# Performance work log

Hardware: AMD Instinct MI355X
Metric: run time of the kernel (lower is better)

Reference implementation:

```python
import jax, jax.numpy as jnp
import numpy as np

TEMPERATURE = 0.5  # init temperature; attn_drop=0.0 so dropout is identity


def setup_inputs() -> dict:
    key = jax.random.key(0)
    k1, k2, k3 = jax.random.split(key, 3)
    B, H, N, D = 4, 8, 2048, 64
    q = jax.random.normal(k1, (B, H, N, D), dtype=jnp.float32)
    k = jax.random.normal(k2, (B, H, N, D), dtype=jnp.float32)
    v = jax.random.normal(k3, (B, H, N, D), dtype=jnp.float32)
    scale = jnp.asarray(D ** -0.5, dtype=jnp.float32)
    return {"q": q, "k": k, "v": v, "scale": scale}


def reference(q, k, v, scale):
    # logits: [B,H,N,N]
    logits = jnp.einsum("bhqd,bhkd->bhqk", q, k) * scale
    # first softmax acts as a soft mask over keys
    soft_mask = jax.nn.softmax(logits / TEMPERATURE, axis=-1)
    # second softmax over masked logits (elementwise product, NOT matmul)
    attn = jax.nn.softmax(logits * soft_mask, axis=-1)
    # dropout with p=0.0 is identity
    out = jnp.einsum("bhqk,bhkd->bhqd", attn, v)
    return out
```

## Files before the change

kernel.cpp:

```cpp
#include <hip/hip_runtime.h>


typedef _Float16 f16;
typedef f16 f16x8 __attribute__((ext_vector_type(8)));
typedef float f32x4 __attribute__((ext_vector_type(4)));

#define MFMA(a, b, c) __builtin_amdgcn_mfma_f32_16x16x32_f16((a), (b), (c), 0, 0, 0)
#define EXP2(x) __builtin_amdgcn_exp2f(x)

#define N_CTX 2048
#define DH 64
#define KT 64
#define NKT (N_CTX / KT)
#define ROWS 128
#define QS 72
#define HEAD_ELEMS (N_CTX * DH)

#define C2 2.885390081777927f

__device__ inline unsigned pk(float a, float b) {
    typedef __fp16 fp16x2_t __attribute__((ext_vector_type(2)));
    union { fp16x2_t v; unsigned u; } x;
    x.v = __builtin_amdgcn_cvt_pkrtz(a, b);
    return x.u;
}

__device__ inline void load16_lds(const f16* g, f16* l) {
    __builtin_amdgcn_global_load_lds(
        (const __attribute__((address_space(1))) void*)g,
        (__attribute__((address_space(3))) void*)l, 16, 0, 0);
}

__global__ __launch_bounds__(256)
void cvt_k(const float* __restrict__ k, f16* __restrict__ out) {
    int i = (blockIdx.x * 256 + threadIdx.x) * 8;
    float4 a = *(const float4*)&k[i];
    float4 b = *(const float4*)&k[i + 4];
    uint4 r = make_uint4(pk(a.x, a.y), pk(a.z, a.w), pk(b.x, b.y), pk(b.z, b.w));
    *(uint4*)&out[i] = r;
}

__global__ __launch_bounds__(256)
void cvt_vt(const float* __restrict__ v, f16* __restrict__ out) {
    __shared__ float Vs[64][65];
    const int bh = blockIdx.x >> 5;
    const int kt = blockIdx.x & 31;
    const int t  = threadIdx.x;
    const float* vb = v + (size_t)bh * HEAD_ELEMS + (size_t)kt * KT * DH;
    #pragma unroll
    for (int it = 0; it < 4; ++it) {
        int idx = it * 256 + t;
        int row = idx >> 4, c4 = idx & 15;
        float4 x = *(const float4*)&vb[row * DH + c4 * 4];
        *(float4*)&Vs[row][c4 * 4] = x;
    }
    __syncthreads();
    int d = t >> 2, kq = t & 3;
    unsigned w[8];
    #pragma unroll
    for (int j = 0; j < 8; ++j)
        w[j] = pk(Vs[kq * 16 + 2 * j][d], Vs[kq * 16 + 2 * j + 1][d]);
    f16* ob = out + (size_t)bh * HEAD_ELEMS + (size_t)d * N_CTX + kt * KT + kq * 16;
    *(uint4*)(ob)     = make_uint4(w[0], w[1], w[2], w[3]);
    *(uint4*)(ob + 8) = make_uint4(w[4], w[5], w[6], w[7]);
}

__global__ __launch_bounds__(512, 4)
void stk_attn_mfma(const float* __restrict__ qg, const f16* __restrict__ kh,
                   const f16* __restrict__ vth, const float* __restrict__ sg,
                   float* __restrict__ og) {
    __shared__ f16 Qs[ROWS * QS];
    __shared__ f16 Ks[2][KT * DH];
    __shared__ f16 Vt[2][DH * KT];
    __shared__ f16 Ps[8][16 * QS];

    const int tid  = threadIdx.x;
    const int wv   = tid >> 6;
    const int lane = tid & 63;
    const int l15  = lane & 15;
    const int q4   = lane >> 4;
    const int bh   = blockIdx.x & 31;
    const int q0   = (blockIdx.x >> 5) * ROWS;
    const float scale2 = sg[0] * C2;

    const float* qb = qg + (size_t)bh * HEAD_ELEMS;
    const f16*   kb = kh + (size_t)bh * HEAD_ELEMS;
    const f16*   vtb = vth + (size_t)bh * HEAD_ELEMS;
    float*       ob = og + (size_t)bh * HEAD_ELEMS;

    #pragma unroll
    for (int it = 0; it < 4; ++it) {
        int idx = it * 512 + tid;
        int row = idx >> 4, c4 = idx & 15;
        float4 v = *(const float4*)&qb[((size_t)(q0 + row)) * DH + c4 * 4];
        *(uint2*)&Qs[row * QS + c4 * 4] =
            make_uint2(pk(v.x * scale2, v.y * scale2), pk(v.z * scale2, v.w * scale2));
    }
    __syncthreads();

    f16x8 aq[2];
    #pragma unroll
    for (int kc = 0; kc < 2; ++kc)
        aq[kc] = *(const f16x8*)&Qs[(wv * 16 + l15) * QS + kc * 32 + q4 * 8];

    const int kc_   = wv * 64 + lane;
    const int kkey  = kc_ >> 3;
    const int kdl   = (kc_ & 7) ^ (kkey & 7);
    const int ks_src = kkey * DH + kdl * 8;
    const long vt_src = (long)kkey * N_CTX + kdl * 8;
    f16* const ks_dst0 = &Ks[0][wv * 512];
    f16* const vt_dst0 = &Vt[0][wv * 512];
    const int ko0 = l15 * 64 + ((q4 ^ (l15 & 7)) * 8);
    const int ko1 = l15 * 64 + (((q4 + 4) ^ (l15 & 7)) * 8);
    const int vo0 = l15 * 64 + ((q4 ^ (l15 & 7)) * 8);
    const int vo1 = l15 * 64 + (((4 + q4) ^ (l15 & 7)) * 8);
    f16* const ps_w = &Ps[wv][(q4 * 4) * QS + l15];
    const f16* const ps_r = &Ps[wv][l15 * QS + q4 * 8];

    float s1[4] = {0, 0, 0, 0};
    load16_lds(kb + ks_src, ks_dst0);
    __syncthreads();
    for (int kt = 0; kt < NKT; ++kt) {
        const int cur = kt & 1;
        if (kt + 1 < NKT)
            load16_lds(kb + (kt + 1) * (KT * DH) + ks_src, ks_dst0 + (cur ^ 1) * (KT * DH));
        #pragma unroll
        for (int kgi = 0; kgi < 4; ++kgi) {
            f16x8 b0 = *(const f16x8*)&Ks[cur][kgi * 1024 + ko0];
            f16x8 b1 = *(const f16x8*)&Ks[cur][kgi * 1024 + ko1];
            f32x4 acc = {0.f, 0.f, 0.f, 0.f};
            acc = MFMA(aq[0], b0, acc);
            acc = MFMA(aq[1], b1, acc);
            #pragma unroll
            for (int r = 0; r < 4; ++r)
                s1[r] += EXP2(acc[r]);
        }
        __syncthreads();
    }
    float inv1[4];
    #pragma unroll
    for (int s = 0; s < 4; ++s) {
        float v = s1[s];
        v += __shfl_xor(v, 1, 64);
        v += __shfl_xor(v, 2, 64);
        v += __shfl_xor(v, 4, 64);
        v += __shfl_xor(v, 8, 64);
        inv1[s] = 0.5f / v;
    }

    float l2[4] = {0, 0, 0, 0};
    f32x4 O[4];
    #pragma unroll
    for (int dt = 0; dt < 4; ++dt) O[dt] = (f32x4){0.f, 0.f, 0.f, 0.f};

    load16_lds(kb + ks_src, ks_dst0);
    load16_lds(vtb + vt_src, vt_dst0);
    __syncthreads();
    for (int kt = 0; kt < NKT; ++kt) {
        const int cur = kt & 1;
        if (kt + 1 < NKT) {
            load16_lds(kb + (kt + 1) * (KT * DH) + ks_src, ks_dst0 + (cur ^ 1) * (KT * DH));
            load16_lds(vtb + vt_src + (kt + 1) * KT, vt_dst0 + (cur ^ 1) * (DH * KT));
        }
        #pragma unroll
        for (int kgi = 0; kgi < 4; ++kgi) {
            f16x8 b0 = *(const f16x8*)&Ks[cur][kgi * 1024 + ko0];
            f16x8 b1 = *(const f16x8*)&Ks[cur][kgi * 1024 + ko1];
            f32x4 acc = {0.f, 0.f, 0.f, 0.f};
            acc = MFMA(aq[0], b0, acc);
            acc = MFMA(aq[1], b1, acc);
            #pragma unroll
            for (int r = 0; r < 4; ++r) {
                float a  = acc[r];
                float e1 = EXP2(a);
                float e2 = EXP2((a * e1) * inv1[r]);
                l2[r] += e2;
                ps_w[r * QS + kgi * 16] = (f16)e2;
            }
        }
        #pragma unroll
        for (int kc = 0; kc < 2; ++kc) {
            f16x8 ap = *(const f16x8*)&ps_r[kc * 32];
            const int vo = (kc == 0) ? vo0 : vo1;
            #pragma unroll
            for (int dt = 0; dt < 4; ++dt) {
                f16x8 bv = *(const f16x8*)&Vt[cur][dt * 1024 + vo];
                O[dt] = MFMA(ap, bv, O[dt]);
            }
        }
        __syncthreads();
    }

    float invl2[4];
    #pragma unroll
    for (int s = 0; s < 4; ++s) {
        float v = l2[s];
        v += __shfl_xor(v, 1, 64);
        v += __shfl_xor(v, 2, 64);
        v += __shfl_xor(v, 4, 64);
        v += __shfl_xor(v, 8, 64);
        invl2[s] = 1.0f / v;
    }
    #pragma unroll
    for (int dt = 0; dt < 4; ++dt)
        #pragma unroll
        for (int r = 0; r < 4; ++r) {
            int row = q0 + wv * 16 + q4 * 4 + r;
            ob[(size_t)row * DH + dt * 16 + l15] = O[dt][r] * invl2[r];
        }
}

extern "C" void kernel_launch(void* const* d_in, const int* in_sizes, int n_in,
                              void* d_out, int out_size, void* d_ws, size_t ws_size,
                              hipStream_t stream) {
    const float* q = (const float*)d_in[0];
    const float* k = (const float*)d_in[1];
    const float* v = (const float*)d_in[2];
    const float* s = (const float*)d_in[3];
    float* out = (float*)d_out;
    f16* kf = (f16*)d_ws;
    f16* vtf = (f16*)((char*)d_ws + 8388608);
    cvt_k<<<2048, 256, 0, stream>>>(k, kf);
    cvt_vt<<<1024, 256, 0, stream>>>(v, vtf);
    dim3 grid(32 * 16);
    stk_attn_mfma<<<grid, 512, 0, stream>>>(q, kf, vtf, s, out);
}
```

Baseline: 175.9 us.

## Switch attention to 32x32x16 MFMA with 4 waves of 32 rows, fuse K/V conversion

Rewrites the main attention kernel to use 32x32x16 MFMA tiles, with each of 4 waves handling 32 query rows instead of 8 waves of 16 rows. This cuts B-operand LDS reads per FLOP and amortizes K/V tile loads over more rows per wave. It also merges the K conversion and V transpose kernels into one launch with a permuted V layout that matches the new P layout. Register pressure rises (16-wide accumulators and per-row statistics), which may reduce occupancy.

```diff
diff --git a/kernel.cpp b/kernel.cpp
--- a/kernel.cpp
+++ b/kernel.cpp
@@ -3,9 +3,9 @@
 
 typedef _Float16 f16;
 typedef f16 f16x8 __attribute__((ext_vector_type(8)));
-typedef float f32x4 __attribute__((ext_vector_type(4)));
-
-#define MFMA(a, b, c) __builtin_amdgcn_mfma_f32_16x16x32_f16((a), (b), (c), 0, 0, 0)
+typedef float f32x16 __attribute__((ext_vector_type(16)));
+
+#define MFMA32(a, b, c) __builtin_amdgcn_mfma_f32_32x32x16_f16((a), (b), (c), 0, 0, 0)
 #define EXP2(x) __builtin_amdgcn_exp2f(x)
 
 #define N_CTX 2048
@@ -15,7 +15,6 @@
 #define ROWS 128
 #define QS 72
 #define HEAD_ELEMS (N_CTX * DH)
-
 #define C2 2.885390081777927f
 
 __device__ inline unsigned pk(float a, float b) {
@@ -32,53 +31,55 @@
 }
 
 __global__ __launch_bounds__(256)
-void cvt_k(const float* __restrict__ k, f16* __restrict__ out) {
-    int i = (blockIdx.x * 256 + threadIdx.x) * 8;
-    float4 a = *(const float4*)&k[i];
-    float4 b = *(const float4*)&k[i + 4];
-    uint4 r = make_uint4(pk(a.x, a.y), pk(a.z, a.w), pk(b.x, b.y), pk(b.z, b.w));
-    *(uint4*)&out[i] = r;
-}
-
-__global__ __launch_bounds__(256)
-void cvt_vt(const float* __restrict__ v, f16* __restrict__ out) {
+void cvt_kv(const float* __restrict__ k, const float* __restrict__ v,
+            f16* __restrict__ ko, f16* __restrict__ vto) {
     __shared__ float Vs[64][65];
-    const int bh = blockIdx.x >> 5;
-    const int kt = blockIdx.x & 31;
+    const int bh = blockIdx.x & 31;
+    const int kt = blockIdx.x >> 5;
     const int t  = threadIdx.x;
+    const float* kb = k + (size_t)bh * HEAD_ELEMS + (size_t)kt * KT * DH;
+    f16* kob = ko + (size_t)bh * HEAD_ELEMS + (size_t)kt * KT * DH;
+    #pragma unroll
+    for (int it = 0; it < 2; ++it) {
+        int i = (it * 256 + t) * 8;
+        float4 a = *(const float4*)&kb[i];
+        float4 b = *(const float4*)&kb[i + 4];
+        *(uint4*)&kob[i] = make_uint4(pk(a.x, a.y), pk(a.z, a.w), pk(b.x, b.y), pk(b.z, b.w));
+    }
     const float* vb = v + (size_t)bh * HEAD_ELEMS + (size_t)kt * KT * DH;
     #pragma unroll
     for (int it = 0; it < 4; ++it) {
         int idx = it * 256 + t;
         int row = idx >> 4, c4 = idx & 15;
-        float4 x = *(const float4*)&vb[row * DH + c4 * 4];
-        *(float4*)&Vs[row][c4 * 4] = x;
-    }
-    __syncthreads();
-    int d = t >> 2, kq = t & 3;
+        *(float4*)&Vs[row][c4 * 4] = *(const float4*)&vb[row * DH + c4 * 4];
+    }
+    __syncthreads();
+    int d = t >> 2, sub = t & 3;
     unsigned w[8];
     #pragma unroll
-    for (int j = 0; j < 8; ++j)
-        w[j] = pk(Vs[kq * 16 + 2 * j][d], Vs[kq * 16 + 2 * j + 1][d]);
-    f16* ob = out + (size_t)bh * HEAD_ELEMS + (size_t)d * N_CTX + kt * KT + kq * 16;
+    for (int j = 0; j < 8; ++j) {
+        int c = sub * 8 + j;
+        w[j] = pk(Vs[c][d], Vs[c + 32][d]);
+    }
+    f16* ob = vto + (size_t)bh * HEAD_ELEMS + (size_t)d * N_CTX + kt * KT + sub * 16;
     *(uint4*)(ob)     = make_uint4(w[0], w[1], w[2], w[3]);
     *(uint4*)(ob + 8) = make_uint4(w[4], w[5], w[6], w[7]);
 }
 
-__global__ __launch_bounds__(512, 4)
+__global__ __launch_bounds__(256, 2)
 void stk_attn_mfma(const float* __restrict__ qg, const f16* __restrict__ kh,
                    const f16* __restrict__ vth, const float* __restrict__ sg,
                    float* __restrict__ og) {
     __shared__ f16 Qs[ROWS * QS];
     __shared__ f16 Ks[2][KT * DH];
     __shared__ f16 Vt[2][DH * KT];
-    __shared__ f16 Ps[8][16 * QS];
+    __shared__ f16 Ps[4][32 * QS];
 
     const int tid  = threadIdx.x;
     const int wv   = tid >> 6;
     const int lane = tid & 63;
-    const int l15  = lane & 15;
-    const int q4   = lane >> 4;
+    const int l31  = lane & 31;
+    const int lh   = lane >> 5;
     const int bh   = blockIdx.x & 31;
     const int q0   = (blockIdx.x >> 5) * ROWS;
     const float scale2 = sg[0] * C2;
@@ -89,8 +90,8 @@
     float*       ob = og + (size_t)bh * HEAD_ELEMS;
 
     #pragma unroll
-    for (int it = 0; it < 4; ++it) {
-        int idx = it * 512 + tid;
+    for (int it = 0; it < 8; ++it) {
+        int idx = it * 256 + tid;
         int row = idx >> 4, c4 = idx & 15;
         float4 v = *(const float4*)&qb[((size_t)(q0 + row)) * DH + c4 * 4];
         *(uint2*)&Qs[row * QS + c4 * 4] =
@@ -98,116 +99,133 @@
     }
     __syncthreads();
 
-    f16x8 aq[2];
-    #pragma unroll
-    for (int kc = 0; kc < 2; ++kc)
-        aq[kc] = *(const f16x8*)&Qs[(wv * 16 + l15) * QS + kc * 32 + q4 * 8];
-
-    const int kc_   = wv * 64 + lane;
-    const int kkey  = kc_ >> 3;
-    const int kdl   = (kc_ & 7) ^ (kkey & 7);
-    const int ks_src = kkey * DH + kdl * 8;
-    const long vt_src = (long)kkey * N_CTX + kdl * 8;
-    f16* const ks_dst0 = &Ks[0][wv * 512];
-    f16* const vt_dst0 = &Vt[0][wv * 512];
-    const int ko0 = l15 * 64 + ((q4 ^ (l15 & 7)) * 8);
-    const int ko1 = l15 * 64 + (((q4 + 4) ^ (l15 & 7)) * 8);
-    const int vo0 = l15 * 64 + ((q4 ^ (l15 & 7)) * 8);
-    const int vo1 = l15 * 64 + (((4 + q4) ^ (l15 & 7)) * 8);
-    f16* const ps_w = &Ps[wv][(q4 * 4) * QS + l15];
-    const f16* const ps_r = &Ps[wv][l15 * QS + q4 * 8];
-
-    float s1[4] = {0, 0, 0, 0};
-    load16_lds(kb + ks_src, ks_dst0);
+    f16x8 aq[4];
+    #pragma unroll
+    for (int km = 0; km < 4; ++km)
+        aq[km] = *(const f16x8*)&Qs[(wv * 32 + l31) * QS + km * 16 + lh * 8];
+
+    const int c0   = (wv * 2) * 64 + lane;
+    const int c1   = c0 + 64;
+    const int key0 = c0 >> 3, key1 = c1 >> 3;
+    const int ks_src0 = key0 * DH + (((c0 & 7) ^ (key0 & 7)) * 8);
+    const int ks_src1 = key1 * DH + (((c1 & 7) ^ (key1 & 7)) * 8);
+    const long vt_src0 = (long)key0 * N_CTX + (((c0 & 7) ^ (key0 & 7)) * 8);
+    const long vt_src1 = (long)key1 * N_CTX + (((c1 & 7) ^ (key1 & 7)) * 8);
+    const int dst0 = (wv * 2) * 512, dst1 = dst0 + 512;
+    const int x8 = l31 & 7;
+    int xo[4];
+    #pragma unroll
+    for (int km = 0; km < 4; ++km) xo[km] = ((2 * km + lh) ^ x8) * 8;
+    const int gb0 = l31 * 64, gb1 = (32 + l31) * 64;
+    f16* const ps_wv = &Ps[wv][0];
+
+    float s1[16] = {0};
+    load16_lds(kb + ks_src0, &Ks[0][dst0]);
+    load16_lds(kb + ks_src1, &Ks[0][dst1]);
     __syncthreads();
     for (int kt = 0; kt < NKT; ++kt) {
         const int cur = kt & 1;
-        if (kt + 1 < NKT)
-            load16_lds(kb + (kt + 1) * (KT * DH) + ks_src, ks_dst0 + (cur ^ 1) * (KT * DH));
-        #pragma unroll
-        for (int kgi = 0; kgi < 4; ++kgi) {
-            f16x8 b0 = *(const f16x8*)&Ks[cur][kgi * 1024 + ko0];
-            f16x8 b1 = *(const f16x8*)&Ks[cur][kgi * 1024 + ko1];
-            f32x4 acc = {0.f, 0.f, 0.f, 0.f};
-            acc = MFMA(aq[0], b0, acc);
-            acc = MFMA(aq[1], b1, acc);
+        if (kt + 1 < NKT) {
+            const f16* src = kb + (kt + 1) * (KT * DH);
+            load16_lds(src + ks_src0, &Ks[cur ^ 1][dst0]);
+            load16_lds(src + ks_src1, &Ks[cur ^ 1][dst1]);
+        }
+        #pragma unroll
+        for (int kg = 0; kg < 2; ++kg) {
+            const int gb = kg ? gb1 : gb0;
+            f32x16 acc;
             #pragma unroll
-            for (int r = 0; r < 4; ++r)
+            for (int i = 0; i < 16; ++i) acc[i] = 0.f;
+            #pragma unroll
+            for (int km = 0; km < 4; ++km) {
+                f16x8 b = *(const f16x8*)&Ks[cur][gb + xo[km]];
+                acc = MFMA32(aq[km], b, acc);
+            }
+            #pragma unroll
+            for (int r = 0; r < 16; ++r)
                 s1[r] += EXP2(acc[r]);
         }
         __syncthreads();
     }
-    float inv1[4];
-    #pragma unroll
-    for (int s = 0; s < 4; ++s) {
-        float v = s1[s];
+    float inv1[16];
+    #pragma unroll
+    for (int r = 0; r < 16; ++r) {
+        float v = s1[r];
         v += __shfl_xor(v, 1, 64);
         v += __shfl_xor(v, 2, 64);
         v += __shfl_xor(v, 4, 64);
         v += __shfl_xor(v, 8, 64);
-        inv1[s] = 0.5f / v;
-    }
-
-    float l2[4] = {0, 0, 0, 0};
-    f32x4 O[4];
-    #pragma unroll
-    for (int dt = 0; dt < 4; ++dt) O[dt] = (f32x4){0.f, 0.f, 0.f, 0.f};
-
-    load16_lds(kb + ks_src, ks_dst0);
-    load16_lds(vtb + vt_src, vt_dst0);
+        v += __shfl_xor(v, 16, 64);
+        inv1[r] = 0.5f / v;
+    }
+
+    float l2[16] = {0};
+    f32x16 O0, O1;
+    #pragma unroll
+    for (int i = 0; i < 16; ++i) { O0[i] = 0.f; O1[i] = 0.f; }
+
+    load16_lds(kb + ks_src0, &Ks[0][dst0]);
+    load16_lds(kb + ks_src1, &Ks[0][dst1]);
+    load16_lds(vtb + vt_src0, &Vt[0][dst0]);
+    load16_lds(vtb + vt_src1, &Vt[0][dst1]);
     __syncthreads();
     for (int kt = 0; kt < NKT; ++kt) {
         const int cur = kt & 1;
         if (kt + 1 < NKT) {
-            load16_lds(kb + (kt + 1) * (KT * DH) + ks_src, ks_dst0 + (cur ^ 1) * (KT * DH));
-            load16_lds(vtb + vt_src + (kt + 1) * KT, vt_dst0 + (cur ^ 1) * (DH * KT));
-        }
-        #pragma unroll
-        for (int kgi = 0; kgi < 4; ++kgi) {
-            f16x8 b0 = *(const f16x8*)&Ks[cur][kgi * 1024 + ko0];
-            f16x8 b1 = *(const f16x8*)&Ks[cur][kgi * 1024 + ko1];
-            f32x4 acc = {0.f, 0.f, 0.f, 0.f};
-            acc = MFMA(aq[0], b0, acc);
-            acc = MFMA(aq[1], b1, acc);
-            #pragma unroll
-            for (int r = 0; r < 4; ++r) {
-                float a  = acc[r];
-                float e1 = EXP2(a);
-                float e2 = EXP2((a * e1) * inv1[r]);
-                l2[r] += e2;
-                ps_w[r * QS + kgi * 16] = (f16)e2;
-            }
-        }
-        #pragma unroll
-        for (int kc = 0; kc < 2; ++kc) {
-            f16x8 ap = *(const f16x8*)&ps_r[kc * 32];
-            const int vo = (kc == 0) ? vo0 : vo1;
-            #pragma unroll
-            for (int dt = 0; dt < 4; ++dt) {
-                f16x8 bv = *(const f16x8*)&Vt[cur][dt * 1024 + vo];
-                O[dt] = MFMA(ap, bv, O[dt]);
-            }
+            const f16* src = kb + (kt + 1) * (KT * DH);
+            load16_lds(src + ks_src0, &Ks[cur ^ 1][dst0]);
+            load16_lds(src + ks_src1, &Ks[cur ^ 1][dst1]);
+            load16_lds(vtb + vt_src0 + (kt + 1) * KT, &Vt[cur ^ 1][dst0]);
+            load16_lds(vtb + vt_src1 + (kt + 1) * KT, &Vt[cur ^ 1][dst1]);
+        }
+        f32x16 a0, a1;
+        #pragma unroll
+        for (int i = 0; i < 16; ++i) { a0[i] = 0.f; a1[i] = 0.f; }
+        #pragma unroll
+        for (int km = 0; km < 4; ++km) {
+            f16x8 b0 = *(const f16x8*)&Ks[cur][gb0 + xo[km]];
+            f16x8 b1 = *(const f16x8*)&Ks[cur][gb1 + xo[km]];
+            a0 = MFMA32(aq[km], b0, a0);
+            a1 = MFMA32(aq[km], b1, a1);
+        }
+        #pragma unroll
+        for (int r = 0; r < 16; ++r) {
+            int row_r = (r & 3) + 8 * (r >> 2) + 4 * lh;
+            float e10 = EXP2(a0[r]);
+            float e20 = EXP2((a0[r] * e10) * inv1[r]);
+            float e11 = EXP2(a1[r]);
+            float e21 = EXP2((a1[r] * e11) * inv1[r]);
+            l2[r] += e20 + e21;
+            *(unsigned*)&ps_wv[row_r * QS + 2 * l31] = pk(e20, e21);
+        }
+        #pragma unroll
+        for (int km = 0; km < 4; ++km) {
+            f16x8 ap = *(const f16x8*)&ps_wv[l31 * QS + km * 16 + lh * 8];
+            f16x8 bv0 = *(const f16x8*)&Vt[cur][gb0 + xo[km]];
+            f16x8 bv1 = *(const f16x8*)&Vt[cur][gb1 + xo[km]];
+            O0 = MFMA32(ap, bv0, O0);
+            O1 = MFMA32(ap, bv1, O1);
         }
         __syncthreads();
     }
 
-    float invl2[4];
-    #pragma unroll
-    for (int s = 0; s < 4; ++s) {
-        float v = l2[s];
+    float invl2[16];
+    #pragma unroll
+    for (int r = 0; r < 16; ++r) {
+        float v = l2[r];
         v += __shfl_xor(v, 1, 64);
         v += __shfl_xor(v, 2, 64);
         v += __shfl_xor(v, 4, 64);
         v += __shfl_xor(v, 8, 64);
-        invl2[s] = 1.0f / v;
-    }
-    #pragma unroll
-    for (int dt = 0; dt < 4; ++dt)
-        #pragma unroll
-        for (int r = 0; r < 4; ++r) {
-            int row = q0 + wv * 16 + q4 * 4 + r;
-            ob[(size_t)row * DH + dt * 16 + l15] = O[dt][r] * invl2[r];
-        }
+        v += __shfl_xor(v, 16, 64);
+        invl2[r] = 1.0f / v;
+    }
+    #pragma unroll
+    for (int r = 0; r < 16; ++r) {
+        int row = q0 + wv * 32 + (r & 3) + 8 * (r >> 2) + 4 * lh;
+        ob[(size_t)row * DH + l31]      = O0[r] * invl2[r];
+        ob[(size_t)row * DH + 32 + l31] = O1[r] * invl2[r];
+    }
 }
 
 extern "C" void kernel_launch(void* const* d_in, const int* in_sizes, int n_in,
@@ -218,10 +236,9 @@
     const float* v = (const float*)d_in[2];
     const float* s = (const float*)d_in[3];
     float* out = (float*)d_out;
-    f16* kf = (f16*)d_ws;
+    f16* kf  = (f16*)d_ws;
     f16* vtf = (f16*)((char*)d_ws + 8388608);
-    cvt_k<<<2048, 256, 0, stream>>>(k, kf);
-    cvt_vt<<<1024, 256, 0, stream>>>(v, vtf);
+    cvt_kv<<<1024, 256, 0, stream>>>(k, v, kf, vtf);
     dim3 grid(32 * 16);
-    stk_attn_mfma<<<grid, 512, 0, stream>>>(q, kf, vtf, s, out);
-}
+    stk_attn_mfma<<<grid, 256, 0, stream>>>(q, kf, vtf, s, out);
+}
```

Result: no change. 177.5 us (+0.9%).

## Software-pipeline QK MFMAs one tile ahead and fuse K/V conversion kernels

Applied to the files above, without the earlier changes.

Both passes now compute the QK^T MFMA tile for the next key block before doing the exp/softmax work on the current one, so matrix-core work overlaps with the transcendental VALU work. K tiles are prefetched two ahead into the double buffer. The separate K-convert and V-transpose kernels are merged into one launch, removing one kernel launch. This costs extra accumulator registers (accN/accC), which may pressure occupancy under launch_bounds(512,4).

```diff
diff --git a/kernel.cpp b/kernel.cpp
--- a/kernel.cpp
+++ b/kernel.cpp
@@ -14,8 +14,8 @@
 #define NKT (N_CTX / KT)
 #define ROWS 128
 #define QS 72
+#define KTDH (KT * DH)
 #define HEAD_ELEMS (N_CTX * DH)
-
 #define C2 2.885390081777927f
 
 __device__ inline unsigned pk(float a, float b) {
@@ -32,35 +32,35 @@
 }
 
 __global__ __launch_bounds__(256)
-void cvt_k(const float* __restrict__ k, f16* __restrict__ out) {
-    int i = (blockIdx.x * 256 + threadIdx.x) * 8;
-    float4 a = *(const float4*)&k[i];
-    float4 b = *(const float4*)&k[i + 4];
-    uint4 r = make_uint4(pk(a.x, a.y), pk(a.z, a.w), pk(b.x, b.y), pk(b.z, b.w));
-    *(uint4*)&out[i] = r;
-}
-
-__global__ __launch_bounds__(256)
-void cvt_vt(const float* __restrict__ v, f16* __restrict__ out) {
+void cvt_kv(const float* __restrict__ k, const float* __restrict__ v,
+            f16* __restrict__ ko, f16* __restrict__ vto) {
     __shared__ float Vs[64][65];
-    const int bh = blockIdx.x >> 5;
-    const int kt = blockIdx.x & 31;
+    const int bh = blockIdx.x & 31;
+    const int kt = blockIdx.x >> 5;
     const int t  = threadIdx.x;
+    const float* kb = k + (size_t)bh * HEAD_ELEMS + (size_t)kt * KT * DH;
+    f16* kob = ko + (size_t)bh * HEAD_ELEMS + (size_t)kt * KT * DH;
+    #pragma unroll
+    for (int it = 0; it < 2; ++it) {
+        int i = (it * 256 + t) * 8;
+        float4 a = *(const float4*)&kb[i];
+        float4 b = *(const float4*)&kb[i + 4];
+        *(uint4*)&kob[i] = make_uint4(pk(a.x, a.y), pk(a.z, a.w), pk(b.x, b.y), pk(b.z, b.w));
+    }
     const float* vb = v + (size_t)bh * HEAD_ELEMS + (size_t)kt * KT * DH;
     #pragma unroll
     for (int it = 0; it < 4; ++it) {
         int idx = it * 256 + t;
         int row = idx >> 4, c4 = idx & 15;
-        float4 x = *(const float4*)&vb[row * DH + c4 * 4];
-        *(float4*)&Vs[row][c4 * 4] = x;
-    }
-    __syncthreads();
-    int d = t >> 2, kq = t & 3;
+        *(float4*)&Vs[row][c4 * 4] = *(const float4*)&vb[row * DH + c4 * 4];
+    }
+    __syncthreads();
+    int d = t >> 2, sub = t & 3;
     unsigned w[8];
     #pragma unroll
     for (int j = 0; j < 8; ++j)
-        w[j] = pk(Vs[kq * 16 + 2 * j][d], Vs[kq * 16 + 2 * j + 1][d]);
-    f16* ob = out + (size_t)bh * HEAD_ELEMS + (size_t)d * N_CTX + kt * KT + kq * 16;
+        w[j] = pk(Vs[sub * 16 + 2 * j][d], Vs[sub * 16 + 2 * j + 1][d]);
+    f16* ob = vto + (size_t)bh * HEAD_ELEMS + (size_t)d * N_CTX + kt * KT + sub * 16;
     *(uint4*)(ob)     = make_uint4(w[0], w[1], w[2], w[3]);
     *(uint4*)(ob + 8) = make_uint4(w[4], w[5], w[6], w[7]);
 }
@@ -70,8 +70,8 @@
                    const f16* __restrict__ vth, const float* __restrict__ sg,
                    float* __restrict__ og) {
     __shared__ f16 Qs[ROWS * QS];
-    __shared__ f16 Ks[2][KT * DH];
-    __shared__ f16 Vt[2][DH * KT];
+    __shared__ f16 Ks[2][KTDH];
+    __shared__ f16 Vt[2][KTDH];
     __shared__ f16 Ps[8][16 * QS];
 
     const int tid  = threadIdx.x;
@@ -83,10 +83,10 @@
     const int q0   = (blockIdx.x >> 5) * ROWS;
     const float scale2 = sg[0] * C2;
 
-    const float* qb = qg + (size_t)bh * HEAD_ELEMS;
-    const f16*   kb = kh + (size_t)bh * HEAD_ELEMS;
+    const float* qb  = qg + (size_t)bh * HEAD_ELEMS;
+    const f16*   kb  = kh + (size_t)bh * HEAD_ELEMS;
     const f16*   vtb = vth + (size_t)bh * HEAD_ELEMS;
-    float*       ob = og + (size_t)bh * HEAD_ELEMS;
+    float*       ob  = og + (size_t)bh * HEAD_ELEMS;
 
     #pragma unroll
     for (int it = 0; it < 4; ++it) {
@@ -103,39 +103,54 @@
     for (int kc = 0; kc < 2; ++kc)
         aq[kc] = *(const f16x8*)&Qs[(wv * 16 + l15) * QS + kc * 32 + q4 * 8];
 
-    const int kc_   = wv * 64 + lane;
-    const int kkey  = kc_ >> 3;
-    const int kdl   = (kc_ & 7) ^ (kkey & 7);
-    const int ks_src = kkey * DH + kdl * 8;
-    const long vt_src = (long)kkey * N_CTX + kdl * 8;
-    f16* const ks_dst0 = &Ks[0][wv * 512];
-    f16* const vt_dst0 = &Vt[0][wv * 512];
+    const int c0   = wv * 64 + lane;
+    const int key0 = c0 >> 3;
+    const int kdl  = (c0 & 7) ^ (key0 & 7);
+    const int ks_src = key0 * DH + kdl * 8;
+    const long vt_src = (long)key0 * N_CTX + kdl * 8;
+    const int dst0 = wv * 512;
     const int ko0 = l15 * 64 + ((q4 ^ (l15 & 7)) * 8);
     const int ko1 = l15 * 64 + (((q4 + 4) ^ (l15 & 7)) * 8);
-    const int vo0 = l15 * 64 + ((q4 ^ (l15 & 7)) * 8);
-    const int vo1 = l15 * 64 + (((4 + q4) ^ (l15 & 7)) * 8);
     f16* const ps_w = &Ps[wv][(q4 * 4) * QS + l15];
     const f16* const ps_r = &Ps[wv][l15 * QS + q4 * 8];
 
     float s1[4] = {0, 0, 0, 0};
-    load16_lds(kb + ks_src, ks_dst0);
-    __syncthreads();
+    f32x4 accC[4], accN[4];
+    load16_lds(kb + ks_src, &Ks[0][dst0]);
+    load16_lds(kb + KTDH + ks_src, &Ks[1][dst0]);
+    __syncthreads();
+    #pragma unroll
+    for (int kgi = 0; kgi < 4; ++kgi) {
+        f16x8 b0 = *(const f16x8*)&Ks[0][kgi * 1024 + ko0];
+        f16x8 b1 = *(const f16x8*)&Ks[0][kgi * 1024 + ko1];
+        f32x4 a = {0.f, 0.f, 0.f, 0.f};
+        a = MFMA(aq[0], b0, a);
+        accC[kgi] = MFMA(aq[1], b1, a);
+    }
+    __syncthreads();
+
     for (int kt = 0; kt < NKT; ++kt) {
-        const int cur = kt & 1;
-        if (kt + 1 < NKT)
-            load16_lds(kb + (kt + 1) * (KT * DH) + ks_src, ks_dst0 + (cur ^ 1) * (KT * DH));
-        #pragma unroll
-        for (int kgi = 0; kgi < 4; ++kgi) {
-            f16x8 b0 = *(const f16x8*)&Ks[cur][kgi * 1024 + ko0];
-            f16x8 b1 = *(const f16x8*)&Ks[cur][kgi * 1024 + ko1];
-            f32x4 acc = {0.f, 0.f, 0.f, 0.f};
-            acc = MFMA(aq[0], b0, acc);
-            acc = MFMA(aq[1], b1, acc);
+        if (kt + 2 < NKT)
+            load16_lds(kb + (kt + 2) * KTDH + ks_src, &Ks[kt & 1][dst0]);
+        if (kt + 1 < NKT) {
+            const f16* ksn = &Ks[(kt + 1) & 1][0];
+            #pragma unroll
+            for (int kgi = 0; kgi < 4; ++kgi) {
+                f16x8 b0 = *(const f16x8*)&ksn[kgi * 1024 + ko0];
+                f16x8 b1 = *(const f16x8*)&ksn[kgi * 1024 + ko1];
+                f32x4 a = {0.f, 0.f, 0.f, 0.f};
+                a = MFMA(aq[0], b0, a);
+                accN[kgi] = MFMA(aq[1], b1, a);
+            }
+        }
+        #pragma unroll
+        for (int kgi = 0; kgi < 4; ++kgi)
             #pragma unroll
             for (int r = 0; r < 4; ++r)
-                s1[r] += EXP2(acc[r]);
-        }
+                s1[r] += EXP2(accC[kgi][r]);
         __syncthreads();
+        #pragma unroll
+        for (int kgi = 0; kgi < 4; ++kgi) accC[kgi] = accN[kgi];
     }
     float inv1[4];
     #pragma unroll
@@ -153,25 +168,41 @@
     #pragma unroll
     for (int dt = 0; dt < 4; ++dt) O[dt] = (f32x4){0.f, 0.f, 0.f, 0.f};
 
-    load16_lds(kb + ks_src, ks_dst0);
-    load16_lds(vtb + vt_src, vt_dst0);
-    __syncthreads();
+    load16_lds(kb + ks_src, &Ks[0][dst0]);
+    load16_lds(kb + KTDH + ks_src, &Ks[1][dst0]);
+    load16_lds(vtb + vt_src, &Vt[0][dst0]);
+    __syncthreads();
+    #pragma unroll
+    for (int kgi = 0; kgi < 4; ++kgi) {
+        f16x8 b0 = *(const f16x8*)&Ks[0][kgi * 1024 + ko0];
+        f16x8 b1 = *(const f16x8*)&Ks[0][kgi * 1024 + ko1];
+        f32x4 a = {0.f, 0.f, 0.f, 0.f};
+        a = MFMA(aq[0], b0, a);
+        accC[kgi] = MFMA(aq[1], b1, a);
+    }
+    __syncthreads();
+
     for (int kt = 0; kt < NKT; ++kt) {
         const int cur = kt & 1;
+        if (kt + 2 < NKT)
+            load16_lds(kb + (kt + 2) * KTDH + ks_src, &Ks[cur][dst0]);
         if (kt + 1 < NKT) {
-            load16_lds(kb + (kt + 1) * (KT * DH) + ks_src, ks_dst0 + (cur ^ 1) * (KT * DH));
-            load16_lds(vtb + vt_src + (kt + 1) * KT, vt_dst0 + (cur ^ 1) * (DH * KT));
+            load16_lds(vtb + vt_src + (kt + 1) * KT, &Vt[cur ^ 1][dst0]);
+            const f16* ksn = &Ks[cur ^ 1][0];
+            #pragma unroll
+            for (int kgi = 0; kgi < 4; ++kgi) {
+                f16x8 b0 = *(const f16x8*)&ksn[kgi * 1024 + ko0];
+                f16x8 b1 = *(const f16x8*)&ksn[kgi * 1024 + ko1];
+                f32x4 a = {0.f, 0.f, 0.f, 0.f};
+                a = MFMA(aq[0], b0, a);
+                accN[kgi] = MFMA(aq[1], b1, a);
+            }
         }
         #pragma unroll
         for (int kgi = 0; kgi < 4; ++kgi) {
-            f16x8 b0 = *(const f16x8*)&Ks[cur][kgi * 1024 + ko0];
-            f16x8 b1 = *(const f16x8*)&Ks[cur][kgi * 1024 + ko1];
-            f32x4 acc = {0.f, 0.f, 0.f, 0.f};
-            acc = MFMA(aq[0], b0, acc);
-            acc = MFMA(aq[1], b1, acc);
             #pragma unroll
             for (int r = 0; r < 4; ++r) {
-                float a  = acc[r];
+                float a  = accC[kgi][r];
                 float e1 = EXP2(a);
                 float e2 = EXP2((a * e1) * inv1[r]);
                 l2[r] += e2;
@@ -181,14 +212,16 @@
         #pragma unroll
         for (int kc = 0; kc < 2; ++kc) {
             f16x8 ap = *(const f16x8*)&ps_r[kc * 32];
-            const int vo = (kc == 0) ? vo0 : vo1;
             #pragma unroll
             for (int dt = 0; dt < 4; ++dt) {
+                int vo = l15 * 64 + (((4 * kc + q4) ^ (l15 & 7)) * 8);
                 f16x8 bv = *(const f16x8*)&Vt[cur][dt * 1024 + vo];
                 O[dt] = MFMA(ap, bv, O[dt]);
             }
         }
         __syncthreads();
+        #pragma unroll
+        for (int kgi = 0; kgi < 4; ++kgi) accC[kgi] = accN[kgi];
     }
 
     float invl2[4];
@@ -218,10 +251,9 @@
     const float* v = (const float*)d_in[2];
     const float* s = (const float*)d_in[3];
     float* out = (float*)d_out;
-    f16* kf = (f16*)d_ws;
+    f16* kf  = (f16*)d_ws;
     f16* vtf = (f16*)((char*)d_ws + 8388608);
-    cvt_k<<<2048, 256, 0, stream>>>(k, kf);
-    cvt_vt<<<1024, 256, 0, stream>>>(v, vtf);
+    cvt_kv<<<1024, 256, 0, stream>>>(k, v, kf, vtf);
     dim3 grid(32 * 16);
     stk_attn_mfma<<<grid, 512, 0, stream>>>(q, kf, vtf, s, out);
 }
```

After: 181.9 us. 1.03x slower.
